# Optimization experiments

Hardware: AMD Instinct MI355X
Metric: run time of the kernel (lower is better)

Reference implementation:

```python
import jax, jax.numpy as jnp
import numpy as np

B, L, CH = 8, 32768, 128   # segments, points per segment, channels
H, D = 4, 32               # num_head, ch_head (CH == H*D)
EPS = 1e-5                 # torch GroupNorm default eps


def group_norm1(x, w, b):
    # GroupNorm(num_groups=1, num_channels=CH) applied on [1, CH, L] per segment:
    # normalize over all channels AND points of each segment, then per-channel affine.
    mu = jnp.mean(x, axis=(1, 2), keepdims=True)            # [B,1,1]
    var = jnp.var(x, axis=(1, 2), keepdims=True)            # [B,1,1]
    return (x - mu) * jax.lax.rsqrt(var + EPS) * w + b      # [B,L,CH]


def setup_inputs() -> dict:
    key = jax.random.key(0)
    k0, k1, k2 = jax.random.split(key, 3)
    x = jax.random.normal(k0, (B, L, CH), dtype=jnp.float32)
    W_qkv = jax.random.normal(k1, (CH, 3 * H * D), dtype=jnp.float32) * 0.02
    W_out = jax.random.normal(k2, (H * D, CH), dtype=jnp.float32) * 0.02
    gn1_w = jnp.ones((CH,), jnp.float32)
    gn1_b = jnp.zeros((CH,), jnp.float32)
    gn2_w = jnp.ones((CH,), jnp.float32)
    gn2_b = jnp.zeros((CH,), jnp.float32)
    return {"x": x, "gn1_w": gn1_w, "gn1_b": gn1_b, "W_qkv": W_qkv,
            "W_out": W_out, "gn2_w": gn2_w, "gn2_b": gn2_b}


def reference(x, gn1_w, gn1_b, W_qkv, W_out, gn2_w, gn2_b):
    norm_x = group_norm1(x, gn1_w, gn1_b)                     # [B,L,CH]
    qkv = norm_x @ W_qkv                                      # [B,L,3*H*D]
    q, k, v = jnp.split(qkv, 3, axis=-1)
    q = q.reshape(B, L, H, D)
    k = k.reshape(B, L, H, D)
    v = v.reshape(B, L, H, D)
    # softmax over points within each segment (k / sqrt(segment_len))
    k_soft = jax.nn.softmax(k * (1.0 / np.float32(np.sqrt(L))), axis=1)
    # per-segment, per-head KV context: [B,H,D,D]
    context = jnp.einsum('blhk,blhv->bhkv', k_soft, v)
    # q scaled by ch_head**-0.5, softmax over feature dim
    q_soft = jax.nn.softmax(q * np.float32(D ** -0.5), axis=-1)
    out = jnp.einsum('blhk,bhkv->blhv', q_soft, context).reshape(B, L, H * D)
    out = out @ W_out                                          # [B,L,CH]
    out = group_norm1(out, gn2_w, gn2_b)
    return out + x  # residual
```

## Files before the change

kernel.cpp:

```cpp
#include <hip/hip_runtime.h>

#define NSEG 8
#define LSEG 32768
#define EPS_GN 1e-5f
#define KSCALE 0.005524271728019903f
#define QSCALE 0.17677669529663687f

typedef __attribute__((ext_vector_type(4))) float f32x4;
typedef __attribute__((ext_vector_type(8))) __bf16 bf16x8;
typedef __attribute__((ext_vector_type(4))) short s16x4;

#define MFMA32(A, B, C) __builtin_amdgcn_mfma_f32_16x16x32_bf16(A, B, C, 0, 0, 0)
#define MFMA16(A, B, C) __builtin_amdgcn_mfma_f32_16x16x16bf16_1k(A, B, C, 0, 0, 0)

static __device__ __forceinline__ unsigned short f2bf(float f) {
  unsigned int u = __float_as_uint(f);
  u += 0x7fffu + ((u >> 16) & 1u);
  return (unsigned short)(u >> 16);
}
static __device__ __forceinline__ float bf2f(unsigned short s) {
  return __uint_as_float(((unsigned int)s) << 16);
}
static __device__ __forceinline__ s16x4 pack4(float a, float b, float c, float d) {
  union { __bf16 h[4]; s16x4 s; } u;
  u.h[0] = (__bf16)a; u.h[1] = (__bf16)b; u.h[2] = (__bf16)c; u.h[3] = (__bf16)d;
  return u.s;
}
static __device__ __forceinline__ s16x4 as_s16x4(ushort4 v) {
  union { ushort4 u; s16x4 s; } c; c.u = v; return c.s;
}

__global__ __launch_bounds__(256) void k_pre(
    const float* __restrict__ x, float* __restrict__ part, unsigned short* __restrict__ xb,
    const float* __restrict__ W, const float* __restrict__ gn1w, unsigned short* __restrict__ WT)
{
  const int t = threadIdx.x;
  if (blockIdx.x >= 512) {
    int idx = (blockIdx.x - 512) * 256 + t;
    int n = idx >> 7, ch = idx & 127;
    WT[idx] = f2bf(gn1w[ch] * W[ch * 384 + n]);
    return;
  }
  const int b = blockIdx.x >> 6, p = blockIdx.x & 63;
  const float4* xp = (const float4*)x + (size_t)b * 1048576 + (size_t)p * 16384;
  ushort4* xo = (ushort4*)xb + (size_t)b * 1048576 + (size_t)p * 16384;
  float s = 0.f, q = 0.f;
  for (int i = 0; i < 64; ++i) {
    float4 v = xp[t + i * 256];
    s += v.x + v.y + v.z + v.w;
    q += v.x*v.x + v.y*v.y + v.z*v.z + v.w*v.w;
    xo[t + i * 256] = make_ushort4(f2bf(v.x), f2bf(v.y), f2bf(v.z), f2bf(v.w));
  }
  #pragma unroll
  for (int o = 1; o < 64; o <<= 1) { s += __shfl_xor(s, o); q += __shfl_xor(q, o); }
  __shared__ float red[8];
  int wave = t >> 6, lane = t & 63;
  if (lane == 0) { red[wave*2] = s; red[wave*2+1] = q; }
  __syncthreads();
  if (t == 0) {
    part[blockIdx.x*2]   = red[0] + red[2] + red[4] + red[6];
    part[blockIdx.x*2+1] = red[1] + red[3] + red[5] + red[7];
  }
}

__global__ void k_bias(const float* __restrict__ Wqkv, const float* __restrict__ gn1w,
                       const float* __restrict__ gn1b, const float* __restrict__ part,
                       float* __restrict__ biasv, float* __restrict__ alpha) {
  const int seg = blockIdx.x, t = threadIdx.x;
  __shared__ float sm[2];
  if (t < 64) {
    float s = part[(seg*64 + t)*2], q = part[(seg*64 + t)*2 + 1];
    #pragma unroll
    for (int o = 1; o < 64; o <<= 1) { s += __shfl_xor(s, o); q += __shfl_xor(q, o); }
    if (t == 0) {
      const float invN = 1.f / 4194304.f;
      float mu = s * invN;
      float var = q * invN - mu * mu;
      sm[0] = mu; sm[1] = rsqrtf(var + EPS_GN);
    }
  }
  __syncthreads();
  const float mu = sm[0], rs = sm[1];
  float s = 0.f;
  for (int ch = 0; ch < 128; ++ch)
    s += (gn1b[ch] - mu * rs * gn1w[ch]) * Wqkv[ch * 384 + t];
  float scale = (t < 128) ? QSCALE : ((t < 256) ? KSCALE : 1.f);
  biasv[seg*384 + t] = s * scale;
  if (t == 0) {
    alpha[seg*4]   = rs * QSCALE;
    alpha[seg*4+1] = rs * KSCALE;
    alpha[seg*4+2] = rs;
  }
}

__global__ __launch_bounds__(256, 2) void k_qkv(
    const unsigned short* __restrict__ xb, const unsigned short* __restrict__ WT,
    const float* __restrict__ biasv, const float* __restrict__ alpha,
    unsigned short* __restrict__ q_ws, float* __restrict__ sume_p, float* __restrict__ ctx_p)
{
  const int t = threadIdx.x;
  const int h = t >> 6, lane = t & 63;
  const int lm = lane & 15, lg = lane >> 4;
  const int bid = blockIdx.x;
  const int seg = bid >> 6, sub = bid & 63;

  bf16x8 wq[2][4], wk[2][4], wv[2][4];
  #pragma unroll
  for (int nt = 0; nt < 2; ++nt)
    #pragma unroll
    for (int kk = 0; kk < 4; ++kk) {
      int row = h*32 + nt*16 + lm;
      wq[nt][kk] = *(const bf16x8*)&WT[(row      ) * 128 + kk*32 + lg*8];
      wk[nt][kk] = *(const bf16x8*)&WT[(row + 128) * 128 + kk*32 + lg*8];
      wv[nt][kk] = *(const bf16x8*)&WT[(row + 256) * 128 + kk*32 + lg*8];
    }
  const float alq = alpha[seg*4], alk = alpha[seg*4 + 1], alv = alpha[seg*4 + 2];
  const float4 cq0 = *(const float4*)&biasv[seg*384 + h*32 +      lg*4];
  const float4 cq1 = *(const float4*)&biasv[seg*384 + h*32 + 16 + lg*4];
  const float ck0 = biasv[seg*384 + 128 + h*32 + lm];
  const float ck1 = biasv[seg*384 + 128 + h*32 + 16 + lm];
  const float cv0 = biasv[seg*384 + 256 + h*32 + lm];
  const float cv1 = biasv[seg*384 + 256 + h*32 + 16 + lm];

  f32x4 ctx00 = {0,0,0,0}, ctx01 = {0,0,0,0}, ctx10 = {0,0,0,0}, ctx11 = {0,0,0,0};
  float se0 = 0.f, se1 = 0.f;

  const unsigned short* xw = xb + (size_t)(seg * LSEG + sub*512 + lm) * 128 + lg*8;
  ushort4* q4 = (ushort4*)q_ws;

#define ISSUE(S, IT) { \
    const unsigned short* p_ = xw + (size_t)((((IT) >> 3) * 128) + (((IT) & 7) * 16)) * 128; \
    S[0] = *(const bf16x8*)(p_);      \
    S[1] = *(const bf16x8*)(p_ + 32); \
    S[2] = *(const bf16x8*)(p_ + 64); \
    S[3] = *(const bf16x8*)(p_ + 96); }

#define COMPUTE(S, IT) { \
    f32x4 qa0 = {0,0,0,0}, qa1 = {0,0,0,0}; \
    _Pragma("unroll") for (int kk = 0; kk < 4; ++kk) { \
      qa0 = MFMA32(wq[0][kk], S[kk], qa0); \
      qa1 = MFMA32(wq[1][kk], S[kk], qa1); \
    } \
    float a_[8]; \
    _Pragma("unroll") for (int r = 0; r < 4; ++r) { \
      a_[r]     = fmaf(qa0[r], alq, ((const float*)&cq0)[r]); \
      a_[4 + r] = fmaf(qa1[r], alq, ((const float*)&cq1)[r]); \
    } \
    float m_ = a_[0]; \
    _Pragma("unroll") for (int i = 1; i < 8; ++i) m_ = fmaxf(m_, a_[i]); \
    m_ = fmaxf(m_, __shfl_xor(m_, 16)); \
    m_ = fmaxf(m_, __shfl_xor(m_, 32)); \
    float s_ = 0.f; \
    _Pragma("unroll") for (int i = 0; i < 8; ++i) { a_[i] = __expf(a_[i] - m_); s_ += a_[i]; } \
    s_ += __shfl_xor(s_, 16); \
    s_ += __shfl_xor(s_, 32); \
    float inv_ = 1.f / s_; \
    { size_t T_ = ((size_t)(bid*4 + ((IT) >> 3))) * 64 + ((IT) & 7) * 8 + h*2; \
      q4[T_*64 + lane]     = make_ushort4(f2bf(a_[0]*inv_), f2bf(a_[1]*inv_), f2bf(a_[2]*inv_), f2bf(a_[3]*inv_)); \
      q4[(T_+1)*64 + lane] = make_ushort4(f2bf(a_[4]*inv_), f2bf(a_[5]*inv_), f2bf(a_[6]*inv_), f2bf(a_[7]*inv_)); } \
    f32x4 ka0 = {0,0,0,0}, ka1 = {0,0,0,0}, va0 = {0,0,0,0}, va1 = {0,0,0,0}; \
    _Pragma("unroll") for (int kk = 0; kk < 4; ++kk) { \
      ka0 = MFMA32(S[kk], wk[0][kk], ka0); \
      ka1 = MFMA32(S[kk], wk[1][kk], ka1); \
    } \
    _Pragma("unroll") for (int kk = 0; kk < 4; ++kk) { \
      va0 = MFMA32(S[kk], wv[0][kk], va0); \
      va1 = MFMA32(S[kk], wv[1][kk], va1); \
    } \
    float e_[8]; \
    _Pragma("unroll") for (int r = 0; r < 4; ++r) { \
      e_[r]     = __expf(fmaf(ka0[r], alk, ck0)); \
      e_[4 + r] = __expf(fmaf(ka1[r], alk, ck1)); \
    } \
    se0 += (e_[0] + e_[1]) + (e_[2] + e_[3]); \
    se1 += (e_[4] + e_[5]) + (e_[6] + e_[7]); \
    s16x4 E0 = pack4(e_[0], e_[1], e_[2], e_[3]); \
    s16x4 E1 = pack4(e_[4], e_[5], e_[6], e_[7]); \
    s16x4 V0 = pack4(fmaf(va0[0], alv, cv0), fmaf(va0[1], alv, cv0), \
                     fmaf(va0[2], alv, cv0), fmaf(va0[3], alv, cv0)); \
    s16x4 V1 = pack4(fmaf(va1[0], alv, cv1), fmaf(va1[1], alv, cv1), \
                     fmaf(va1[2], alv, cv1), fmaf(va1[3], alv, cv1)); \
    ctx00 = MFMA16(E0, V0, ctx00); \
    ctx01 = MFMA16(E0, V1, ctx01); \
    ctx10 = MFMA16(E1, V0, ctx10); \
    ctx11 = MFMA16(E1, V1, ctx11); }

  bf16x8 sA[4], sB[4], sC[4], sD[4];
  ISSUE(sA, 0);
  ISSUE(sB, 1);
  #pragma unroll 1
  for (int it = 0; it < 32; it += 4) {
    ISSUE(sC, it + 2);
    COMPUTE(sA, it);
    ISSUE(sD, it + 3);
    COMPUTE(sB, it + 1);
    if (it + 4 < 32) ISSUE(sA, it + 4);
    COMPUTE(sC, it + 2);
    if (it + 5 < 32) ISSUE(sB, it + 5);
    COMPUTE(sD, it + 3);
  }
#undef ISSUE
#undef COMPUTE

  se0 += __shfl_xor(se0, 16); se0 += __shfl_xor(se0, 32);
  se1 += __shfl_xor(se1, 16); se1 += __shfl_xor(se1, 32);
  if (lane < 16) {
    sume_p[(size_t)bid*128 + h*32 + lm]      = se0;
    sume_p[(size_t)bid*128 + h*32 + 16 + lm] = se1;
  }
  float* cp = ctx_p + (size_t)bid*4096 + h*1024;
  #pragma unroll
  for (int r = 0; r < 4; ++r) {
    cp[(lg*4 + r)*32      + lm]      = ctx00[r];
    cp[(lg*4 + r)*32      + 16 + lm] = ctx01[r];
    cp[(16 + lg*4 + r)*32 + lm]      = ctx10[r];
    cp[(16 + lg*4 + r)*32 + 16 + lm] = ctx11[r];
  }
}

__global__ __launch_bounds__(512) void k_ctx_final(
    const float* __restrict__ sume_p, const float* __restrict__ ctx_p,
    const float* __restrict__ Wout, unsigned short* __restrict__ WcT)
{
  __shared__ float sse[128];
  __shared__ float sctx[4096];
  __shared__ float sWo[16384];
  const int t = threadIdx.x, b = blockIdx.x;
  if (t < 128) {
    float s = 0.f;
    for (int blk = 0; blk < 64; ++blk) s += sume_p[(size_t)(b * 64 + blk) * 128 + t];
    sse[t] = s;
  }
  float cv[8];
  #pragma unroll
  for (int j = 0; j < 8; ++j) {
    int idx = t + j * 512;
    float s = 0.f;
    for (int blk = 0; blk < 64; ++blk) s += ctx_p[(size_t)(b * 64 + blk) * 4096 + idx];
    cv[j] = s;
  }
  #pragma unroll
  for (int j = 0; j < 32; ++j) sWo[t + j * 512] = Wout[t + j * 512];
  __syncthreads();
  #pragma unroll
  for (int j = 0; j < 8; ++j) {
    int idx = t + j * 512;
    sctx[idx] = cv[j] / sse[idx >> 5];
  }
  __syncthreads();
  const int p = t >> 2, c0 = (t & 3) * 32;
  const int h = p >> 5;
  float acc[32];
  #pragma unroll
  for (int j = 0; j < 32; ++j) acc[j] = 0.f;
  for (int v = 0; v < 32; ++v) {
    float a = sctx[p * 32 + v];
    const float* wr = &sWo[(h * 32 + v) * 128 + c0];
    #pragma unroll
    for (int j = 0; j < 32; ++j) acc[j] += a * wr[j];
  }
  #pragma unroll
  for (int j = 0; j < 32; ++j)
    WcT[((size_t)b * 128 + (c0 + j)) * 128 + p] = f2bf(acc[j]);
}

__global__ __launch_bounds__(512) void k_out(
    unsigned short* __restrict__ q_ws, const unsigned short* __restrict__ WcT,
    float* __restrict__ stats2_p)
{
  __shared__ __attribute__((aligned(16))) unsigned short sWc[128 * 136];
  __shared__ __attribute__((aligned(16))) unsigned char sO[8][16 * 272];
  __shared__ float red[16];

  const int t = threadIdx.x, wave = t >> 6, lane = t & 63;
  const int lm = lane & 15, lg = lane >> 4;
  const int bid = blockIdx.x;
  const int seg = bid >> 8;

  const ushort4* q4c = (const ushort4*)q_ws;
  s16x4 p[8];
  #pragma unroll
  for (int kt = 0; kt < 8; ++kt)
    p[kt] = as_s16x4(q4c[((size_t)bid * 64 + wave * 8 + kt) * 64 + lane]);

  const ushort4* wc4 = (const ushort4*)WcT + (size_t)seg * 4096;
  #pragma unroll
  for (int i = 0; i < 8; ++i) {
    int f = t + i * 512;
    *(ushort4*)&sWc[(f >> 5) * 136 + (f & 31) * 4] = wc4[f];
  }
  __syncthreads();

  float ssum = 0.f, ssq = 0.f;
  unsigned char* so = &sO[wave][0];
  #pragma unroll
  for (int ot = 0; ot < 8; ++ot) {
    f32x4 acc = {0,0,0,0};
    #pragma unroll
    for (int kt = 0; kt < 8; ++kt) {
      s16x4 wf = *(const s16x4*)&sWc[(ot*16 + lm) * 136 + kt*16 + lg*4];
      acc = MFMA16(wf, p[kt], acc);
    }
    #pragma unroll
    for (int r = 0; r < 4; ++r) { ssum += acc[r]; ssq += acc[r] * acc[r]; }
    *(ushort4*)(so + lm * 272 + ot * 32 + lg * 8) =
        make_ushort4(f2bf(acc[0]), f2bf(acc[1]), f2bf(acc[2]), f2bf(acc[3]));
  }
  #pragma unroll
  for (int i = 0; i < 4; ++i) {
    int row = i * 4 + (lane >> 4);
    float4 v = *(const float4*)(so + row * 272 + (lane & 15) * 16);
    *(float4*)((char*)q_ws + ((size_t)bid * 128 + wave * 16 + row) * 256 + (lane & 15) * 16) = v;
  }

  #pragma unroll
  for (int o = 1; o < 64; o <<= 1) { ssum += __shfl_xor(ssum, o); ssq += __shfl_xor(ssq, o); }
  if (lane == 0) { red[wave*2] = ssum; red[wave*2+1] = ssq; }
  __syncthreads();
  if (t == 0) {
    float s = 0.f, q = 0.f;
    #pragma unroll
    for (int w = 0; w < 8; ++w) { s += red[w*2]; q += red[w*2+1]; }
    stats2_p[bid*2] = s; stats2_p[bid*2+1] = q;
  }
}

__global__ __launch_bounds__(256) void k_final(
    const unsigned short* __restrict__ xb, const unsigned short* __restrict__ out_ws,
    const float* __restrict__ stats2_p, const float* __restrict__ gn2w, const float* __restrict__ gn2b,
    float* __restrict__ y)
{
  __shared__ float red[8];
  __shared__ float sm[2];
  const int t = threadIdx.x;
  const int b = blockIdx.x >> 8, blk = blockIdx.x & 255;
  {
    float s = stats2_p[(b*256 + t)*2], q = stats2_p[(b*256 + t)*2 + 1];
    #pragma unroll
    for (int o = 1; o < 64; o <<= 1) { s += __shfl_xor(s, o); q += __shfl_xor(q, o); }
    int wave = t >> 6, lane = t & 63;
    if (lane == 0) { red[wave*2] = s; red[wave*2+1] = q; }
    __syncthreads();
    if (t == 0) {
      float ss = red[0] + red[2] + red[4] + red[6];
      float qq = red[1] + red[3] + red[5] + red[7];
      const float invN = 1.f / 4194304.f;
      float mu = ss * invN;
      float var = qq * invN - mu * mu;
      sm[0] = mu; sm[1] = rsqrtf(var + EPS_GN);
    }
    __syncthreads();
  }
  const float mu = sm[0], rs = sm[1];
  const int c4 = t & 31;
  const float4 w4 = *(const float4*)&gn2w[c4*4];
  const float4 g4 = *(const float4*)&gn2b[c4*4];
  const size_t base = (size_t)b * 1048576 + (size_t)blk * 4096;
  const ushort4* xp = (const ushort4*)xb + base;
  const ushort4* op = (const ushort4*)out_ws + base;
  float4* yp = (float4*)y + base;
  #pragma unroll
  for (int i = 0; i < 16; ++i) {
    int f = t + i * 256;
    ushort4 xv = xp[f];
    ushort4 ov = op[f];
    float4 r;
    r.x = (bf2f(ov.x) - mu) * rs * w4.x + g4.x + bf2f(xv.x);
    r.y = (bf2f(ov.y) - mu) * rs * w4.y + g4.y + bf2f(xv.y);
    r.z = (bf2f(ov.z) - mu) * rs * w4.z + g4.z + bf2f(xv.z);
    r.w = (bf2f(ov.w) - mu) * rs * w4.w + g4.w + bf2f(xv.w);
    yp[f] = r;
  }
}

extern "C" void kernel_launch(void* const* d_in, const int* in_sizes, int n_in,
                              void* d_out, int out_size, void* d_ws, size_t ws_size,
                              hipStream_t stream) {
  const float* x    = (const float*)d_in[0];
  const float* gn1w = (const float*)d_in[1];
  const float* gn1b = (const float*)d_in[2];
  const float* Wqkv = (const float*)d_in[3];
  const float* Wout = (const float*)d_in[4];
  const float* gn2w = (const float*)d_in[5];
  const float* gn2b = (const float*)d_in[6];
  float* y = (float*)d_out;
  char* ws = (char*)d_ws;

  float*          part    = (float*)(ws + 0);
  unsigned short* WT      = (unsigned short*)(ws + 8192);
  float*          biasv   = (float*)(ws + 106496);
  float*          alphav  = (float*)(ws + 118784);
  float*          sume_p  = (float*)(ws + 122880);
  float*          ctx_p   = (float*)(ws + 385024);
  unsigned short* WcT     = (unsigned short*)(ws + 8773632);
  float*          stats2p = (float*)(ws + 9035776);
  unsigned short* xb      = (unsigned short*)(ws + 9052160);
  unsigned short* q_ws    = (unsigned short*)(ws + 76161024);

  hipLaunchKernelGGL(k_pre,       dim3(704),  dim3(256), 0, stream, x, part, xb, Wqkv, gn1w, WT);
  hipLaunchKernelGGL(k_bias,      dim3(8),    dim3(384), 0, stream, Wqkv, gn1w, gn1b, part, biasv, alphav);
  hipLaunchKernelGGL(k_qkv,       dim3(512),  dim3(256), 0, stream, xb, WT, biasv, alphav, q_ws, sume_p, ctx_p);
  hipLaunchKernelGGL(k_ctx_final, dim3(8),    dim3(512), 0, stream, sume_p, ctx_p, Wout, WcT);
  hipLaunchKernelGGL(k_out,       dim3(2048), dim3(512), 0, stream, q_ws, WcT, stats2p);
  hipLaunchKernelGGL(k_final,     dim3(2048), dim3(256), 0, stream, xb, q_ws, stats2p, gn2w, gn2b, y);
}
```

Measured before the change: 211.1 us.

## Recompute Q in output pass and fuse GroupNorm2 via cooperative grid sync

Q projection and softmax move out of the KV pass into the output kernel, which recomputes them from bf16 x, so the q workspace is never written or reread. The bias setup kernel is folded into the consuming kernels, and the context reduction is split across 256 blocks instead of 8. The output kernel holds its bf16 results in registers, syncs the grid cooperatively to get the second GroupNorm statistics, then writes y directly, which removes the out round trip and the separate final kernel. Risks are high register pressure from holding 32x2 outputs per thread, extra MFMA work, per-step block barriers, and a fallback path if the cooperative launch fails.

```diff
diff --git a/kernel.cpp b/kernel.cpp
--- a/kernel.cpp
+++ b/kernel.cpp
@@ -1,10 +1,14 @@
 #include <hip/hip_runtime.h>
+#include <hip/hip_cooperative_groups.h>
+
+namespace cg = cooperative_groups;
 
 #define NSEG 8
 #define LSEG 32768
 #define EPS_GN 1e-5f
 #define KSCALE 0.005524271728019903f
 #define QSCALE 0.17677669529663687f
+#define INVN 2.384185791015625e-07f
 
 typedef __attribute__((ext_vector_type(4))) float f32x4;
 typedef __attribute__((ext_vector_type(8))) __bf16 bf16x8;
@@ -26,8 +30,10 @@
   u.h[0] = (__bf16)a; u.h[1] = (__bf16)b; u.h[2] = (__bf16)c; u.h[3] = (__bf16)d;
   return u.s;
 }
-static __device__ __forceinline__ s16x4 as_s16x4(ushort4 v) {
-  union { ushort4 u; s16x4 s; } c; c.u = v; return c.s;
+static __device__ __forceinline__ uint2 packo(f32x4 v) {
+  union { unsigned short h[4]; uint2 u; } z;
+  z.h[0] = f2bf(v[0]); z.h[1] = f2bf(v[1]); z.h[2] = f2bf(v[2]); z.h[3] = f2bf(v[3]);
+  return z.u;
 }
 
 __global__ __launch_bounds__(256) void k_pre(
@@ -41,9 +47,9 @@
     WT[idx] = f2bf(gn1w[ch] * W[ch * 384 + n]);
     return;
   }
-  const int b = blockIdx.x >> 6, p = blockIdx.x & 63;
-  const float4* xp = (const float4*)x + (size_t)b * 1048576 + (size_t)p * 16384;
-  ushort4* xo = (ushort4*)xb + (size_t)b * 1048576 + (size_t)p * 16384;
+  const int c = blockIdx.x;
+  const float4* xp = (const float4*)x + (size_t)c * 16384;
+  ushort4* xo = (ushort4*)xb + (size_t)c * 16384;
   float s = 0.f, q = 0.f;
   for (int i = 0; i < 64; ++i) {
     float4 v = xp[t + i * 256];
@@ -58,106 +64,81 @@
   if (lane == 0) { red[wave*2] = s; red[wave*2+1] = q; }
   __syncthreads();
   if (t == 0) {
-    part[blockIdx.x*2]   = red[0] + red[2] + red[4] + red[6];
-    part[blockIdx.x*2+1] = red[1] + red[3] + red[5] + red[7];
-  }
-}
-
-__global__ void k_bias(const float* __restrict__ Wqkv, const float* __restrict__ gn1w,
-                       const float* __restrict__ gn1b, const float* __restrict__ part,
-                       float* __restrict__ biasv, float* __restrict__ alpha) {
-  const int seg = blockIdx.x, t = threadIdx.x;
+    part[c*2]   = red[0] + red[2] + red[4] + red[6];
+    part[c*2+1] = red[1] + red[3] + red[5] + red[7];
+  }
+}
+
+__global__ __launch_bounds__(256, 2) void k_kv(
+    const unsigned short* __restrict__ xb, const unsigned short* __restrict__ WT,
+    const float* __restrict__ Wqkv, const float* __restrict__ gn1w, const float* __restrict__ gn1b,
+    const float* __restrict__ part, float* __restrict__ sume_p, float* __restrict__ ctx_p)
+{
   __shared__ float sm[2];
-  if (t < 64) {
-    float s = part[(seg*64 + t)*2], q = part[(seg*64 + t)*2 + 1];
-    #pragma unroll
-    for (int o = 1; o < 64; o <<= 1) { s += __shfl_xor(s, o); q += __shfl_xor(q, o); }
-    if (t == 0) {
-      const float invN = 1.f / 4194304.f;
-      float mu = s * invN;
-      float var = q * invN - mu * mu;
-      sm[0] = mu; sm[1] = rsqrtf(var + EPS_GN);
-    }
-  }
-  __syncthreads();
-  const float mu = sm[0], rs = sm[1];
-  float s = 0.f;
-  for (int ch = 0; ch < 128; ++ch)
-    s += (gn1b[ch] - mu * rs * gn1w[ch]) * Wqkv[ch * 384 + t];
-  float scale = (t < 128) ? QSCALE : ((t < 256) ? KSCALE : 1.f);
-  biasv[seg*384 + t] = s * scale;
-  if (t == 0) {
-    alpha[seg*4]   = rs * QSCALE;
-    alpha[seg*4+1] = rs * KSCALE;
-    alpha[seg*4+2] = rs;
-  }
-}
-
-__global__ __launch_bounds__(256, 2) void k_qkv(
-    const unsigned short* __restrict__ xb, const unsigned short* __restrict__ WT,
-    const float* __restrict__ biasv, const float* __restrict__ alpha,
-    unsigned short* __restrict__ q_ws, float* __restrict__ sume_p, float* __restrict__ ctx_p)
-{
+  __shared__ float sb01[512];
+  __shared__ float sbias[256];
+
   const int t = threadIdx.x;
   const int h = t >> 6, lane = t & 63;
   const int lm = lane & 15, lg = lane >> 4;
   const int bid = blockIdx.x;
   const int seg = bid >> 6, sub = bid & 63;
 
-  bf16x8 wq[2][4], wk[2][4], wv[2][4];
+  if (t < 64) {
+    float s = part[(seg*64 + t)*2], q = part[(seg*64 + t)*2 + 1];
+    #pragma unroll
+    for (int o = 1; o < 64; o <<= 1) { s += __shfl_xor(s, o); q += __shfl_xor(q, o); }
+    if (t == 0) {
+      float mu = s * INVN;
+      float var = q * INVN - mu * mu;
+      float rs = rsqrtf(var + EPS_GN);
+      sm[0] = mu * rs; sm[1] = rs;
+    }
+  }
+  for (int p = t; p < 512; p += 256) {
+    int which = p >> 8, n = 128 + (p & 255);
+    const float* gv = which ? gn1w : gn1b;
+    float s = 0.f;
+    for (int ch = 0; ch < 128; ++ch) s += gv[ch] * Wqkv[ch*384 + n];
+    sb01[p] = s;
+  }
+  __syncthreads();
+  {
+    float mu_rs = sm[0];
+    int p = t;
+    float v = sb01[p] - mu_rs * sb01[256 + p];
+    sbias[p] = v * ((p < 128) ? KSCALE : 1.f);
+  }
+  __syncthreads();
+
+  const float rs = sm[1];
+  const float alk = rs * KSCALE, alv = rs;
+  const float ck0 = sbias[h*32 + lm],       ck1 = sbias[h*32 + 16 + lm];
+  const float cv0 = sbias[128 + h*32 + lm], cv1 = sbias[128 + h*32 + 16 + lm];
+
+  bf16x8 wk[2][4], wv[2][4];
   #pragma unroll
   for (int nt = 0; nt < 2; ++nt)
     #pragma unroll
     for (int kk = 0; kk < 4; ++kk) {
       int row = h*32 + nt*16 + lm;
-      wq[nt][kk] = *(const bf16x8*)&WT[(row      ) * 128 + kk*32 + lg*8];
       wk[nt][kk] = *(const bf16x8*)&WT[(row + 128) * 128 + kk*32 + lg*8];
       wv[nt][kk] = *(const bf16x8*)&WT[(row + 256) * 128 + kk*32 + lg*8];
     }
-  const float alq = alpha[seg*4], alk = alpha[seg*4 + 1], alv = alpha[seg*4 + 2];
-  const float4 cq0 = *(const float4*)&biasv[seg*384 + h*32 +      lg*4];
-  const float4 cq1 = *(const float4*)&biasv[seg*384 + h*32 + 16 + lg*4];
-  const float ck0 = biasv[seg*384 + 128 + h*32 + lm];
-  const float ck1 = biasv[seg*384 + 128 + h*32 + 16 + lm];
-  const float cv0 = biasv[seg*384 + 256 + h*32 + lm];
-  const float cv1 = biasv[seg*384 + 256 + h*32 + 16 + lm];
 
   f32x4 ctx00 = {0,0,0,0}, ctx01 = {0,0,0,0}, ctx10 = {0,0,0,0}, ctx11 = {0,0,0,0};
   float se0 = 0.f, se1 = 0.f;
 
   const unsigned short* xw = xb + (size_t)(seg * LSEG + sub*512 + lm) * 128 + lg*8;
-  ushort4* q4 = (ushort4*)q_ws;
 
 #define ISSUE(S, IT) { \
-    const unsigned short* p_ = xw + (size_t)((((IT) >> 3) * 128) + (((IT) & 7) * 16)) * 128; \
+    const unsigned short* p_ = xw + (size_t)((IT) * 16) * 128; \
     S[0] = *(const bf16x8*)(p_);      \
     S[1] = *(const bf16x8*)(p_ + 32); \
     S[2] = *(const bf16x8*)(p_ + 64); \
     S[3] = *(const bf16x8*)(p_ + 96); }
 
-#define COMPUTE(S, IT) { \
-    f32x4 qa0 = {0,0,0,0}, qa1 = {0,0,0,0}; \
-    _Pragma("unroll") for (int kk = 0; kk < 4; ++kk) { \
-      qa0 = MFMA32(wq[0][kk], S[kk], qa0); \
-      qa1 = MFMA32(wq[1][kk], S[kk], qa1); \
-    } \
-    float a_[8]; \
-    _Pragma("unroll") for (int r = 0; r < 4; ++r) { \
-      a_[r]     = fmaf(qa0[r], alq, ((const float*)&cq0)[r]); \
-      a_[4 + r] = fmaf(qa1[r], alq, ((const float*)&cq1)[r]); \
-    } \
-    float m_ = a_[0]; \
-    _Pragma("unroll") for (int i = 1; i < 8; ++i) m_ = fmaxf(m_, a_[i]); \
-    m_ = fmaxf(m_, __shfl_xor(m_, 16)); \
-    m_ = fmaxf(m_, __shfl_xor(m_, 32)); \
-    float s_ = 0.f; \
-    _Pragma("unroll") for (int i = 0; i < 8; ++i) { a_[i] = __expf(a_[i] - m_); s_ += a_[i]; } \
-    s_ += __shfl_xor(s_, 16); \
-    s_ += __shfl_xor(s_, 32); \
-    float inv_ = 1.f / s_; \
-    { size_t T_ = ((size_t)(bid*4 + ((IT) >> 3))) * 64 + ((IT) & 7) * 8 + h*2; \
-      q4[T_*64 + lane]     = make_ushort4(f2bf(a_[0]*inv_), f2bf(a_[1]*inv_), f2bf(a_[2]*inv_), f2bf(a_[3]*inv_)); \
-      q4[(T_+1)*64 + lane] = make_ushort4(f2bf(a_[4]*inv_), f2bf(a_[5]*inv_), f2bf(a_[6]*inv_), f2bf(a_[7]*inv_)); } \
+#define COMPUTE(S) { \
     f32x4 ka0 = {0,0,0,0}, ka1 = {0,0,0,0}, va0 = {0,0,0,0}, va1 = {0,0,0,0}; \
     _Pragma("unroll") for (int kk = 0; kk < 4; ++kk) { \
       ka0 = MFMA32(S[kk], wk[0][kk], ka0); \
@@ -191,13 +172,13 @@
   #pragma unroll 1
   for (int it = 0; it < 32; it += 4) {
     ISSUE(sC, it + 2);
-    COMPUTE(sA, it);
+    COMPUTE(sA);
     ISSUE(sD, it + 3);
-    COMPUTE(sB, it + 1);
+    COMPUTE(sB);
     if (it + 4 < 32) ISSUE(sA, it + 4);
-    COMPUTE(sC, it + 2);
+    COMPUTE(sC);
     if (it + 5 < 32) ISSUE(sB, it + 5);
-    COMPUTE(sD, it + 3);
+    COMPUTE(sD);
   }
 #undef ISSUE
 #undef COMPUTE
@@ -218,139 +199,263 @@
   }
 }
 
-__global__ __launch_bounds__(512) void k_ctx_final(
+__global__ __launch_bounds__(256) void k_wc(
     const float* __restrict__ sume_p, const float* __restrict__ ctx_p,
     const float* __restrict__ Wout, unsigned short* __restrict__ WcT)
 {
-  __shared__ float sse[128];
-  __shared__ float sctx[4096];
-  __shared__ float sWo[16384];
+  __shared__ float sctx[1024];
+  __shared__ float sse[32];
   const int t = threadIdx.x, b = blockIdx.x;
-  if (t < 128) {
+  const int seg = b >> 5, head = (b >> 3) & 3, ocg = b & 7;
+  float acc[4] = {0.f, 0.f, 0.f, 0.f};
+  for (int j = 0; j < 64; ++j) {
+    const float* cp = ctx_p + (size_t)(seg*64 + j)*4096 + head*1024;
+    #pragma unroll
+    for (int e = 0; e < 4; ++e) acc[e] += cp[t + e*256];
+  }
+  if (t < 32) {
     float s = 0.f;
-    for (int blk = 0; blk < 64; ++blk) s += sume_p[(size_t)(b * 64 + blk) * 128 + t];
+    for (int j = 0; j < 64; ++j) s += sume_p[(size_t)(seg*64 + j)*128 + head*32 + t];
     sse[t] = s;
   }
-  float cv[8];
-  #pragma unroll
-  for (int j = 0; j < 8; ++j) {
-    int idx = t + j * 512;
+  #pragma unroll
+  for (int e = 0; e < 4; ++e) sctx[t + e*256] = acc[e];
+  __syncthreads();
+  #pragma unroll
+  for (int e = 0; e < 2; ++e) {
+    int idx = t + e*256;
+    int kc = idx >> 4, ocl = idx & 15;
+    int oc = ocg*16 + ocl;
     float s = 0.f;
-    for (int blk = 0; blk < 64; ++blk) s += ctx_p[(size_t)(b * 64 + blk) * 4096 + idx];
-    cv[j] = s;
-  }
-  #pragma unroll
-  for (int j = 0; j < 32; ++j) sWo[t + j * 512] = Wout[t + j * 512];
-  __syncthreads();
-  #pragma unroll
-  for (int j = 0; j < 8; ++j) {
-    int idx = t + j * 512;
-    sctx[idx] = cv[j] / sse[idx >> 5];
-  }
-  __syncthreads();
-  const int p = t >> 2, c0 = (t & 3) * 32;
-  const int h = p >> 5;
-  float acc[32];
-  #pragma unroll
-  for (int j = 0; j < 32; ++j) acc[j] = 0.f;
-  for (int v = 0; v < 32; ++v) {
-    float a = sctx[p * 32 + v];
-    const float* wr = &sWo[(h * 32 + v) * 128 + c0];
-    #pragma unroll
-    for (int j = 0; j < 32; ++j) acc[j] += a * wr[j];
-  }
-  #pragma unroll
-  for (int j = 0; j < 32; ++j)
-    WcT[((size_t)b * 128 + (c0 + j)) * 128 + p] = f2bf(acc[j]);
-}
-
-__global__ __launch_bounds__(512) void k_out(
-    unsigned short* __restrict__ q_ws, const unsigned short* __restrict__ WcT,
-    float* __restrict__ stats2_p)
+    #pragma unroll
+    for (int vc = 0; vc < 32; ++vc)
+      s += sctx[kc*32 + vc] * Wout[(head*32 + vc)*128 + oc];
+    WcT[((size_t)seg*128 + oc)*128 + head*32 + kc] = f2bf(s / sse[kc]);
+  }
+}
+
+template<bool COOP>
+__global__ __launch_bounds__(256, 2) void k_out2(
+    const unsigned short* __restrict__ xb, const unsigned short* __restrict__ WT,
+    const float* __restrict__ Wqkv, const float* __restrict__ gn1w, const float* __restrict__ gn1b,
+    const float* __restrict__ part, const unsigned short* __restrict__ WcT,
+    const float* __restrict__ gn2w, const float* __restrict__ gn2b,
+    float* __restrict__ part2, unsigned short* __restrict__ outm, float* __restrict__ y)
 {
-  __shared__ __attribute__((aligned(16))) unsigned short sWc[128 * 136];
-  __shared__ __attribute__((aligned(16))) unsigned char sO[8][16 * 272];
-  __shared__ float red[16];
-
-  const int t = threadIdx.x, wave = t >> 6, lane = t & 63;
+  __shared__ float sm[2];
+  __shared__ float sb01[256];
+  __shared__ float sbq[128];
+  __shared__ float red[8];
+  __shared__ float sm2[8][2];
+  __shared__ float sgw[128], sgb[128];
+  __shared__ __attribute__((aligned(16))) short pbuf[2][8 * 256];
+  __shared__ __attribute__((aligned(16))) float sOf[2][16 * 136];
+
+  const int t = threadIdx.x;
+  const int w = t >> 6, lane = t & 63;
   const int lm = lane & 15, lg = lane >> 4;
   const int bid = blockIdx.x;
-  const int seg = bid >> 8;
-
-  const ushort4* q4c = (const ushort4*)q_ws;
-  s16x4 p[8];
-  #pragma unroll
-  for (int kt = 0; kt < 8; ++kt)
-    p[kt] = as_s16x4(q4c[((size_t)bid * 64 + wave * 8 + kt) * 64 + lane]);
-
-  const ushort4* wc4 = (const ushort4*)WcT + (size_t)seg * 4096;
-  #pragma unroll
-  for (int i = 0; i < 8; ++i) {
-    int f = t + i * 512;
-    *(ushort4*)&sWc[(f >> 5) * 136 + (f & 31) * 4] = wc4[f];
-  }
-  __syncthreads();
-
+  const int seg = bid >> 6;
+  const size_t cb = (size_t)bid * 512;
+
+  if (t < 64) {
+    float s = part[(seg*64 + t)*2], q = part[(seg*64 + t)*2 + 1];
+    #pragma unroll
+    for (int o = 1; o < 64; o <<= 1) { s += __shfl_xor(s, o); q += __shfl_xor(q, o); }
+    if (t == 0) {
+      float mu = s * INVN;
+      float var = q * INVN - mu * mu;
+      float rs = rsqrtf(var + EPS_GN);
+      sm[0] = mu * rs; sm[1] = rs;
+    }
+  }
+  for (int p = t; p < 256; p += 256) {
+    int which = p >> 7, n = p & 127;
+    const float* gv = which ? gn1w : gn1b;
+    float s = 0.f;
+    for (int ch = 0; ch < 128; ++ch) s += gv[ch] * Wqkv[ch*384 + n];
+    sb01[p] = s;
+  }
+  if (t < 128) { sgw[t] = gn2w[t]; sgb[t] = gn2b[t]; }
+  __syncthreads();
+  if (t < 128) sbq[t] = (sb01[t] - sm[0] * sb01[128 + t]) * QSCALE;
+  __syncthreads();
+
+  const float alq = sm[1] * QSCALE;
+  const float4 cq0 = *(const float4*)&sbq[w*32 + lg*4];
+  const float4 cq1 = *(const float4*)&sbq[w*32 + 16 + lg*4];
+
+  bf16x8 wq[2][4];
+  #pragma unroll
+  for (int nt = 0; nt < 2; ++nt)
+    #pragma unroll
+    for (int kk = 0; kk < 4; ++kk)
+      wq[nt][kk] = *(const bf16x8*)&WT[(w*32 + nt*16 + lm) * 128 + kk*32 + lg*8];
+  s16x4 wc[2][8];
+  #pragma unroll
+  for (int o = 0; o < 2; ++o)
+    #pragma unroll
+    for (int kt = 0; kt < 8; ++kt)
+      wc[o][kt] = *(const s16x4*)&WcT[((size_t)seg*128 + (w*32 + o*16 + lm))*128 + kt*16 + lg*4];
+
+  const unsigned short* xw = xb + (cb + lm) * 128 + lg*8;
+  uint2 oreg[32][2];
   float ssum = 0.f, ssq = 0.f;
-  unsigned char* so = &sO[wave][0];
-  #pragma unroll
-  for (int ot = 0; ot < 8; ++ot) {
-    f32x4 acc = {0,0,0,0};
+
+  #pragma unroll
+  for (int ia = 0; ia < 32; ++ia) {
+    const unsigned short* p_ = xw + (size_t)(ia * 16) * 128;
+    bf16x8 xf0 = *(const bf16x8*)(p_);
+    bf16x8 xf1 = *(const bf16x8*)(p_ + 32);
+    bf16x8 xf2 = *(const bf16x8*)(p_ + 64);
+    bf16x8 xf3 = *(const bf16x8*)(p_ + 96);
+    f32x4 qa0 = {0,0,0,0}, qa1 = {0,0,0,0};
+    qa0 = MFMA32(wq[0][0], xf0, qa0); qa1 = MFMA32(wq[1][0], xf0, qa1);
+    qa0 = MFMA32(wq[0][1], xf1, qa0); qa1 = MFMA32(wq[1][1], xf1, qa1);
+    qa0 = MFMA32(wq[0][2], xf2, qa0); qa1 = MFMA32(wq[1][2], xf2, qa1);
+    qa0 = MFMA32(wq[0][3], xf3, qa0); qa1 = MFMA32(wq[1][3], xf3, qa1);
+    float a[8];
+    #pragma unroll
+    for (int r = 0; r < 4; ++r) {
+      a[r]     = fmaf(qa0[r], alq, ((const float*)&cq0)[r]);
+      a[4 + r] = fmaf(qa1[r], alq, ((const float*)&cq1)[r]);
+    }
+    float m = a[0];
+    #pragma unroll
+    for (int i = 1; i < 8; ++i) m = fmaxf(m, a[i]);
+    m = fmaxf(m, __shfl_xor(m, 16));
+    m = fmaxf(m, __shfl_xor(m, 32));
+    float s = 0.f;
+    #pragma unroll
+    for (int i = 0; i < 8; ++i) { a[i] = __expf(a[i] - m); s += a[i]; }
+    s += __shfl_xor(s, 16);
+    s += __shfl_xor(s, 32);
+    float inv = 1.f / s;
+    *(s16x4*)&pbuf[ia & 1][(w*2)*256 + lane*4]     = pack4(a[0]*inv, a[1]*inv, a[2]*inv, a[3]*inv);
+    *(s16x4*)&pbuf[ia & 1][(w*2 + 1)*256 + lane*4] = pack4(a[4]*inv, a[5]*inv, a[6]*inv, a[7]*inv);
+    __syncthreads();
+    f32x4 acc0 = {0,0,0,0}, acc1 = {0,0,0,0};
     #pragma unroll
     for (int kt = 0; kt < 8; ++kt) {
-      s16x4 wf = *(const s16x4*)&sWc[(ot*16 + lm) * 136 + kt*16 + lg*4];
-      acc = MFMA16(wf, p[kt], acc);
-    }
-    #pragma unroll
-    for (int r = 0; r < 4; ++r) { ssum += acc[r]; ssq += acc[r] * acc[r]; }
-    *(ushort4*)(so + lm * 272 + ot * 32 + lg * 8) =
-        make_ushort4(f2bf(acc[0]), f2bf(acc[1]), f2bf(acc[2]), f2bf(acc[3]));
-  }
-  #pragma unroll
-  for (int i = 0; i < 4; ++i) {
-    int row = i * 4 + (lane >> 4);
-    float4 v = *(const float4*)(so + row * 272 + (lane & 15) * 16);
-    *(float4*)((char*)q_ws + ((size_t)bid * 128 + wave * 16 + row) * 256 + (lane & 15) * 16) = v;
+      s16x4 pk = *(const s16x4*)&pbuf[ia & 1][kt*256 + lane*4];
+      acc0 = MFMA16(wc[0][kt], pk, acc0);
+      acc1 = MFMA16(wc[1][kt], pk, acc1);
+    }
+    #pragma unroll
+    for (int r = 0; r < 4; ++r) {
+      ssum += acc0[r] + acc1[r];
+      ssq  += acc0[r]*acc0[r] + acc1[r]*acc1[r];
+    }
+    if constexpr (COOP) {
+      oreg[ia][0] = packo(acc0);
+      oreg[ia][1] = packo(acc1);
+    } else {
+      unsigned short* sou = (unsigned short*)&sOf[0][0];
+      uint2 v0 = packo(acc0), v1 = packo(acc1);
+      unsigned short* dst = &sou[lm*272 + w*32 + lg*4];
+      dst[0] = (unsigned short)(v0.x & 0xffff); dst[1] = (unsigned short)(v0.x >> 16);
+      dst[2] = (unsigned short)(v0.y & 0xffff); dst[3] = (unsigned short)(v0.y >> 16);
+      dst += 16;
+      dst[0] = (unsigned short)(v1.x & 0xffff); dst[1] = (unsigned short)(v1.x >> 16);
+      dst[2] = (unsigned short)(v1.y & 0xffff); dst[3] = (unsigned short)(v1.y >> 16);
+      __syncthreads();
+      #pragma unroll
+      for (int j = 0; j < 2; ++j) {
+        int f = t + j*256;
+        int pt = f >> 5, cc = f & 31;
+        ((ushort4*)outm)[(cb + (size_t)ia*16 + pt)*32 + cc] = *(const ushort4*)&sou[pt*272 + cc*4];
+      }
+      __syncthreads();
+    }
   }
 
   #pragma unroll
   for (int o = 1; o < 64; o <<= 1) { ssum += __shfl_xor(ssum, o); ssq += __shfl_xor(ssq, o); }
-  if (lane == 0) { red[wave*2] = ssum; red[wave*2+1] = ssq; }
+  if (lane == 0) { red[w*2] = ssum; red[w*2+1] = ssq; }
   __syncthreads();
   if (t == 0) {
-    float s = 0.f, q = 0.f;
-    #pragma unroll
-    for (int w = 0; w < 8; ++w) { s += red[w*2]; q += red[w*2+1]; }
-    stats2_p[bid*2] = s; stats2_p[bid*2+1] = q;
-  }
-}
-
-__global__ __launch_bounds__(256) void k_final(
+    part2[bid*2]   = red[0] + red[2] + red[4] + red[6];
+    part2[bid*2+1] = red[1] + red[3] + red[5] + red[7];
+  }
+
+  if constexpr (!COOP) return;
+
+  __threadfence();
+  cg::this_grid().sync();
+
+  {
+    int l = t & 63;
+    for (int sseg = w; sseg < 8; sseg += 4) {
+      float s = part2[(sseg*64 + l)*2], q = part2[(sseg*64 + l)*2 + 1];
+      #pragma unroll
+      for (int o = 1; o < 64; o <<= 1) { s += __shfl_xor(s, o); q += __shfl_xor(q, o); }
+      if (l == 0) {
+        float mu = s * INVN;
+        float var = q * INVN - mu * mu;
+        sm2[sseg][0] = mu; sm2[sseg][1] = rsqrtf(var + EPS_GN);
+      }
+    }
+  }
+  __syncthreads();
+  const float mu2 = sm2[seg][0], rs2 = sm2[seg][1];
+  const int c4 = t & 31;
+  const float4 w4 = *(const float4*)&sgw[c4*4];
+  const float4 g4 = *(const float4*)&sgb[c4*4];
+  const ushort4* xb4 = (const ushort4*)xb;
+  float4* y4 = (float4*)y;
+
+  #pragma unroll
+  for (int ia = 0; ia < 32; ++ia) {
+    float* so = &sOf[ia & 1][0];
+    {
+      uint2 v0 = oreg[ia][0], v1 = oreg[ia][1];
+      float* dst = &so[lm*136 + w*32 + lg*4];
+      dst[0] = bf2f((unsigned short)(v0.x & 0xffff));
+      dst[1] = bf2f((unsigned short)(v0.x >> 16));
+      dst[2] = bf2f((unsigned short)(v0.y & 0xffff));
+      dst[3] = bf2f((unsigned short)(v0.y >> 16));
+      dst += 16;
+      dst[0] = bf2f((unsigned short)(v1.x & 0xffff));
+      dst[1] = bf2f((unsigned short)(v1.x >> 16));
+      dst[2] = bf2f((unsigned short)(v1.y & 0xffff));
+      dst[3] = bf2f((unsigned short)(v1.y >> 16));
+    }
+    __syncthreads();
+    #pragma unroll
+    for (int j = 0; j < 2; ++j) {
+      int f = t + j*256;
+      int pt = f >> 5, cc = f & 31;
+      float4 ov = *(const float4*)&so[pt*136 + cc*4];
+      ushort4 xv = xb4[(cb + (size_t)ia*16 + pt)*32 + cc];
+      float4 r;
+      r.x = (ov.x - mu2) * rs2 * w4.x + g4.x + bf2f(xv.x);
+      r.y = (ov.y - mu2) * rs2 * w4.y + g4.y + bf2f(xv.y);
+      r.z = (ov.z - mu2) * rs2 * w4.z + g4.z + bf2f(xv.z);
+      r.w = (ov.w - mu2) * rs2 * w4.w + g4.w + bf2f(xv.w);
+      y4[(cb + (size_t)ia*16 + pt)*32 + cc] = r;
+    }
+  }
+}
+
+__global__ __launch_bounds__(256) void k_final_old(
     const unsigned short* __restrict__ xb, const unsigned short* __restrict__ out_ws,
-    const float* __restrict__ stats2_p, const float* __restrict__ gn2w, const float* __restrict__ gn2b,
+    const float* __restrict__ part2, const float* __restrict__ gn2w, const float* __restrict__ gn2b,
     float* __restrict__ y)
 {
-  __shared__ float red[8];
   __shared__ float sm[2];
   const int t = threadIdx.x;
   const int b = blockIdx.x >> 8, blk = blockIdx.x & 255;
-  {
-    float s = stats2_p[(b*256 + t)*2], q = stats2_p[(b*256 + t)*2 + 1];
+  if (t < 64) {
+    float s = part2[(b*64 + t)*2], q = part2[(b*64 + t)*2 + 1];
     #pragma unroll
     for (int o = 1; o < 64; o <<= 1) { s += __shfl_xor(s, o); q += __shfl_xor(q, o); }
-    int wave = t >> 6, lane = t & 63;
-    if (lane == 0) { red[wave*2] = s; red[wave*2+1] = q; }
-    __syncthreads();
     if (t == 0) {
-      float ss = red[0] + red[2] + red[4] + red[6];
-      float qq = red[1] + red[3] + red[5] + red[7];
-      const float invN = 1.f / 4194304.f;
-      float mu = ss * invN;
-      float var = qq * invN - mu * mu;
+      float mu = s * INVN;
+      float var = q * INVN - mu * mu;
       sm[0] = mu; sm[1] = rsqrtf(var + EPS_GN);
     }
-    __syncthreads();
-  }
+  }
+  __syncthreads();
   const float mu = sm[0], rs = sm[1];
   const int c4 = t & 31;
   const float4 w4 = *(const float4*)&gn2w[c4*4];
@@ -386,21 +491,34 @@
   float* y = (float*)d_out;
   char* ws = (char*)d_ws;
 
-  float*          part    = (float*)(ws + 0);
-  unsigned short* WT      = (unsigned short*)(ws + 8192);
-  float*          biasv   = (float*)(ws + 106496);
-  float*          alphav  = (float*)(ws + 118784);
-  float*          sume_p  = (float*)(ws + 122880);
-  float*          ctx_p   = (float*)(ws + 385024);
-  unsigned short* WcT     = (unsigned short*)(ws + 8773632);
-  float*          stats2p = (float*)(ws + 9035776);
-  unsigned short* xb      = (unsigned short*)(ws + 9052160);
-  unsigned short* q_ws    = (unsigned short*)(ws + 76161024);
-
-  hipLaunchKernelGGL(k_pre,       dim3(704),  dim3(256), 0, stream, x, part, xb, Wqkv, gn1w, WT);
-  hipLaunchKernelGGL(k_bias,      dim3(8),    dim3(384), 0, stream, Wqkv, gn1w, gn1b, part, biasv, alphav);
-  hipLaunchKernelGGL(k_qkv,       dim3(512),  dim3(256), 0, stream, xb, WT, biasv, alphav, q_ws, sume_p, ctx_p);
-  hipLaunchKernelGGL(k_ctx_final, dim3(8),    dim3(512), 0, stream, sume_p, ctx_p, Wout, WcT);
-  hipLaunchKernelGGL(k_out,       dim3(2048), dim3(512), 0, stream, q_ws, WcT, stats2p);
-  hipLaunchKernelGGL(k_final,     dim3(2048), dim3(256), 0, stream, xb, q_ws, stats2p, gn2w, gn2b, y);
-}
+  float*          part   = (float*)(ws + 0);
+  float*          part2  = (float*)(ws + 4096);
+  unsigned short* WT     = (unsigned short*)(ws + 8192);
+  unsigned short* WcT    = (unsigned short*)(ws + 106496);
+  float*          sume_p = (float*)(ws + 368640);
+  float*          ctx_p  = (float*)(ws + 630784);
+  unsigned short* xb     = (unsigned short*)(ws + 9019392);
+  unsigned short* outm   = (unsigned short*)(ws + 76128256);
+
+  hipLaunchKernelGGL(k_pre, dim3(704), dim3(256), 0, stream, x, part, xb, Wqkv, gn1w, WT);
+  hipLaunchKernelGGL(k_kv,  dim3(512), dim3(256), 0, stream, xb, WT, Wqkv, gn1w, gn1b, part, sume_p, ctx_p);
+  hipLaunchKernelGGL(k_wc,  dim3(256), dim3(256), 0, stream, sume_p, ctx_p, Wout, WcT);
+
+  const unsigned short* xb_c  = xb;
+  const unsigned short* WT_c  = WT;
+  const unsigned short* WcT_c = WcT;
+  const float* part_c = part;
+  void* args[] = {
+    (void*)&xb_c, (void*)&WT_c, (void*)&Wqkv, (void*)&gn1w, (void*)&gn1b,
+    (void*)&part_c, (void*)&WcT_c, (void*)&gn2w, (void*)&gn2b,
+    (void*)&part2, (void*)&outm, (void*)&y
+  };
+  hipError_t ce = hipLaunchCooperativeKernel((void*)k_out2<true>, dim3(512), dim3(256),
+                                             args, 0, stream);
+  if (ce != hipSuccess) {
+    hipLaunchKernelGGL((k_out2<false>), dim3(512), dim3(256), 0, stream,
+                       xb, WT, Wqkv, gn1w, gn1b, part, WcT, gn2w, gn2b, part2, outm, y);
+    hipLaunchKernelGGL(k_final_old, dim3(2048), dim3(256), 0, stream,
+                       xb, outm, part2, gn2w, gn2b, y);
+  }
+}
```

Result: slower. 302.0 us (+43.1%).
